# Performance work log

Measured on AMD Instinct MI355X. Metric: run time of the kernel, lower is better.

## Reference

```python
import jax, jax.numpy as jnp
import numpy as np

D_MODEL = 1024
N_HEAD = 16
HEAD_DIM = D_MODEL // N_HEAD
D_INNER = (int(D_MODEL * 2.0) + 7) // 8 * 8  # 2048
EPS = 1e-6


def setup_inputs() -> dict:
    key = jax.random.key(0)
    ks = jax.random.split(key, 8)
    B, T = 2, 2048
    s = 0.02
    return {
        "x": jax.random.normal(ks[0], (B, T, D_MODEL), dtype=jnp.float32),
        "ln1_w": jnp.ones((D_MODEL,), jnp.float32),
        "ln2_w": jnp.ones((D_MODEL,), jnp.float32),
        "qkv_w": jax.random.normal(ks[1], (3 * D_MODEL, D_MODEL), jnp.float32) * s,
        "o_w": jax.random.normal(ks[2], (D_MODEL, D_MODEL), jnp.float32) * s,
        "gate_w": jax.random.normal(ks[3], (D_INNER, D_MODEL), jnp.float32) * s,
        "up_w": jax.random.normal(ks[4], (D_INNER, D_MODEL), jnp.float32) * s,
        "down_w": jax.random.normal(ks[5], (D_MODEL, D_INNER), jnp.float32) * s,
    }


def _rmsnorm(x, w):
    xf = x.astype(jnp.float32)
    rms = jax.lax.rsqrt(jnp.mean(xf * xf, axis=-1, keepdims=True) + EPS)
    return (xf * rms).astype(x.dtype) * w


def _attention(x, qkv_w, o_w):
    B, T, D = x.shape
    qkv = (x @ qkv_w.T).reshape(B, T, 3, N_HEAD, HEAD_DIM)
    q, k, v = qkv[:, :, 0], qkv[:, :, 1], qkv[:, :, 2]  # [B,T,H,hd]
    scale = 1.0 / np.sqrt(HEAD_DIM)
    att = jnp.einsum("bqhd,bkhd->bhqk", q, k) * scale
    causal = jnp.tril(jnp.ones((T, T), dtype=bool))
    att = jnp.where(causal[None, None], att, -jnp.inf)
    att = jax.nn.softmax(att, axis=-1)
    y = jnp.einsum("bhqk,bkhd->bqhd", att, v).reshape(B, T, D)
    return y @ o_w.T


def _ffn(x, gate_w, up_w, down_w):
    g = jax.nn.silu(x @ gate_w.T)
    u = x @ up_w.T
    return (g * u) @ down_w.T


def reference(x, ln1_w, ln2_w, qkv_w, o_w, gate_w, up_w, down_w):
    x = x + _attention(_rmsnorm(x, ln1_w), qkv_w, o_w)
    x = x + _ffn(_rmsnorm(x, ln2_w), gate_w, up_w, down_w)
    return x
```

## Files before the change

kernel.cpp:

```cpp
#include <hip/hip_runtime.h>
#include <hip/hip_bf16.h>
#include <cstdint>

typedef __hip_bfloat16 bf16;
typedef __attribute__((ext_vector_type(8))) short bf16x8;
typedef __attribute__((ext_vector_type(4))) float f32x4;
typedef __attribute__((ext_vector_type(4))) int i32x4;

#define T_SEQ 2048
#define DMODEL 1024
#define NHEAD 16
#define DHEAD 64
#define MROWS 4096

typedef const __attribute__((address_space(1))) void* gas_ptr;
typedef __attribute__((address_space(3))) void* las_ptr;

static __device__ __forceinline__ f32x4 mfma16(bf16x8 a, bf16x8 b, f32x4 c) {
  return __builtin_amdgcn_mfma_f32_16x16x32_bf16(a, b, c, 0, 0, 0);
}
static __device__ __forceinline__ void gload_lds16(const void* g, void* l) {
  __builtin_amdgcn_global_load_lds((gas_ptr)g, (las_ptr)l, 16, 0, 0);
}
static __device__ __forceinline__ float b2f(unsigned short u) {
  union { unsigned int i; float f; } x; x.i = ((unsigned int)u) << 16; return x.f;
}
static __device__ __forceinline__ unsigned short f2bu(float f) {
  __hip_bfloat16 h = __float2bfloat16(f);
  unsigned short u; __builtin_memcpy(&u, &h, 2); return u;
}

__global__ __launch_bounds__(256) void f2ball_k(const float* __restrict__ a,
                                                const float* __restrict__ b,
                                                const float* __restrict__ c,
                                                const float* __restrict__ d,
                                                const float* __restrict__ e,
                                                bf16* __restrict__ out) {
  const int idx = (blockIdx.x * 256 + threadIdx.x) * 4;
  const float* src;
  int off;
  if (idx < 3145728)      { src = a; off = idx; }
  else if (idx < 4194304) { src = b; off = idx - 3145728; }
  else if (idx < 6291456) { src = c; off = idx - 4194304; }
  else if (idx < 8388608) { src = d; off = idx - 6291456; }
  else                    { src = e; off = idx - 8388608; }
  const float4 v = *(const float4*)(src + off);
  ushort4 ov;
  ov.x = f2bu(v.x); ov.y = f2bu(v.y); ov.z = f2bu(v.z); ov.w = f2bu(v.w);
  *(ushort4*)((unsigned short*)out + idx) = ov;
}

__global__ __launch_bounds__(256) void rms_k(const float* __restrict__ x,
                                             const float* __restrict__ w,
                                             bf16* __restrict__ out) {
  const int row = blockIdx.x;
  const int tid = threadIdx.x;
  const float4 v = ((const float4*)(x + (size_t)row * DMODEL))[tid];
  float ss = v.x * v.x + v.y * v.y + v.z * v.z + v.w * v.w;
#pragma unroll
  for (int off = 32; off; off >>= 1) ss += __shfl_xor(ss, off);
  __shared__ float red[4];
  if ((tid & 63) == 0) red[tid >> 6] = ss;
  __syncthreads();
  const float tot = red[0] + red[1] + red[2] + red[3];
  const float rinv = rsqrtf(tot * (1.f / DMODEL) + 1e-6f);
  const float4 wv = ((const float4*)w)[tid];
  bf16* o = out + (size_t)row * DMODEL + tid * 4;
  o[0] = __float2bfloat16(v.x * rinv * wv.x);
  o[1] = __float2bfloat16(v.y * rinv * wv.y);
  o[2] = __float2bfloat16(v.z * rinv * wv.z);
  o[3] = __float2bfloat16(v.w * rinv * wv.w);
}

template <int K, int EPI>
__global__ __launch_bounds__(256) void gemm_bt(const bf16* __restrict__ A,
                                               const bf16* __restrict__ Bw, int N,
                                               void* __restrict__ o0, void* __restrict__ o1,
                                               void* __restrict__ o2,
                                               const float* __restrict__ res) {
  __shared__ bf16 As[128 * 32];
  __shared__ bf16 Bs[128 * 32];
  const int bn0 = blockIdx.x * 128;
  const int bm0 = blockIdx.y * 128;
  const int tid = threadIdx.x;
  const int wave = tid >> 6, lane = tid & 63;
  const int wr = wave >> 1, wc = wave & 1;
  const int fr = lane & 15, g8 = (lane >> 4) * 8, r4 = (lane >> 4) * 4;
  const int srow = lane >> 2;
  const int scol = (lane & 3) * 8;

  const f32x4 fzero = {0.f, 0.f, 0.f, 0.f};
  f32x4 acc[4][4];
#pragma unroll
  for (int i = 0; i < 4; i++)
#pragma unroll
    for (int j = 0; j < 4; j++) acc[i][j] = fzero;

  const bf16* gA0 = A + (size_t)(bm0 + wave * 16 + srow) * K + scol;
  const bf16* gA1 = A + (size_t)(bm0 + (wave + 4) * 16 + srow) * K + scol;
  const bf16* gB0 = Bw + (size_t)(bn0 + wave * 16 + srow) * K + scol;
  const bf16* gB1 = Bw + (size_t)(bn0 + (wave + 4) * 16 + srow) * K + scol;

  for (int k0 = 0; k0 < K; k0 += 32) {
    gload_lds16(gA0 + k0, &As[wave * 512]);
    gload_lds16(gA1 + k0, &As[(wave + 4) * 512]);
    gload_lds16(gB0 + k0, &Bs[wave * 512]);
    gload_lds16(gB1 + k0, &Bs[(wave + 4) * 512]);
    __syncthreads();
    bf16x8 af[4], bfr[4];
#pragma unroll
    for (int mr = 0; mr < 4; mr++)
      af[mr] = *(const bf16x8*)&As[(wr * 64 + mr * 16 + fr) * 32 + g8];
#pragma unroll
    for (int nr = 0; nr < 4; nr++)
      bfr[nr] = *(const bf16x8*)&Bs[(wc * 64 + nr * 16 + fr) * 32 + g8];
#pragma unroll
    for (int mr = 0; mr < 4; mr++)
#pragma unroll
      for (int nr = 0; nr < 4; nr++)
        acc[mr][nr] = mfma16(af[mr], bfr[nr], acc[mr][nr]);
    __syncthreads();
  }

#pragma unroll
  for (int mr = 0; mr < 4; mr++) {
#pragma unroll
    for (int nr = 0; nr < 4; nr++) {
#pragma unroll
      for (int r = 0; r < 4; r++) {
        const int row = bm0 + wr * 64 + mr * 16 + r4 + r;
        const int col = bn0 + wc * 64 + nr * 16 + fr;
        const float vsum = acc[mr][nr][r];
        if (EPI == 0) {
          ((bf16*)o0)[(size_t)row * N + col] = __float2bfloat16(vsum);
        } else if (EPI == 1) {
          const int sel = col >> 10;
          const int n = col & 1023;
          const int h = n >> 6, d = n & 63;
          const int b = row >> 11, t = row & 2047;
          if (sel == 2) {
            ((bf16*)o2)[(((size_t)(b * NHEAD + h)) * DHEAD + d) * T_SEQ + t] =
                __float2bfloat16(vsum);
          } else {
            bf16* dst = (sel == 0) ? (bf16*)o0 : (bf16*)o1;
            dst[(((size_t)(b * NHEAD + h)) * T_SEQ + t) * DHEAD + d] = __float2bfloat16(vsum);
          }
        } else if (EPI == 2) {
          ((float*)o0)[(size_t)row * N + col] = res[(size_t)row * N + col] + vsum;
        } else {
          const int half = N >> 1;
          bf16* dst = (col < half) ? (bf16*)o0 : (bf16*)o1;
          const int c = (col < half) ? col : col - half;
          dst[(size_t)row * half + c] = __float2bfloat16(vsum);
        }
      }
    }
  }
}

__global__ __launch_bounds__(256) void attn_k(const bf16* __restrict__ qb,
                                              const bf16* __restrict__ kb,
                                              const bf16* __restrict__ vt,
                                              bf16* __restrict__ y,
                                              unsigned short* __restrict__ pO,
                                              float* __restrict__ pL) {
  const int wave = threadIdx.x >> 6, lane = threadIdx.x & 63;
  const int bid = blockIdx.x;
  int bh, qt, ks0, nb, heavy, hs;
  if (bid < 1024) {
    const int c = bid & 7, r = bid >> 3;
    bh = c * 4 + (r & 3);
    const int idx = r >> 2;
    qt = 31 - (idx >> 1);
    hs = idx & 1;
    heavy = 1;
    nb = qt + 1;
    ks0 = hs * nb;
  } else {
    const int bd = bid - 1024;
    const int c = bd & 7, r = bd >> 3;
    bh = c * 4 + (r & 3);
    qt = 15 - (r >> 2);
    hs = 0;
    heavy = 0;
    nb = 2 * qt + 2;
    ks0 = 0;
  }
  const int b = bh >> 4, h = bh & 15;
  const int fr = lane & 15, g8 = (lane >> 4) * 8, r4 = (lane >> 4) * 4;
  const int u = lane >> 4;
  const int src1 = fr + ((u & 1) << 5);
  const int src2 = src1 + 16;
  const bool hB = u >= 2;

  const bf16* qp = qb + (size_t)bh * T_SEQ * DHEAD;
  const bf16* kp = kb + (size_t)bh * T_SEQ * DHEAD;
  const bf16* vp = vt + (size_t)bh * DHEAD * T_SEQ;

  __shared__ char Ks[2][4096];
  __shared__ char Vs[2][4096];

  const int q0 = qt * 64 + wave * 16;
  const int kend = q0 + 16;
  const int qrow = q0 + fr;

  const bf16x8 qf0 = *(const bf16x8*)(qp + (size_t)(q0 + fr) * DHEAD + g8);
  const bf16x8 qf1 = *(const bf16x8*)(qp + (size_t)(q0 + fr) * DHEAD + 32 + g8);

  const int krow_l = lane >> 3;
  const int kslot_l = (lane & 7) ^ krow_l;
  const int vrow_l = lane >> 2;
  const int vslot_l = (lane & 3) ^ ((lane >> 3) & 3);

  const int kswz = (fr & 7) << 4;
  const int koffA = fr * 128 + ((u * 16) ^ kswz);
  const int koffB = fr * 128 + (((4 + u) * 16) ^ kswz);
  const int vswz = ((fr >> 1) & 3) << 4;

  const f32x4 fzero = {0.f, 0.f, 0.f, 0.f};
  f32x4 acc[4];
  float lpart = 0.f;
#pragma unroll
  for (int nf = 0; nf < 4; nf++) acc[nf] = fzero;

  gload_lds16(kp + (size_t)(ks0 * 32 + wave * 8 + krow_l) * DHEAD + kslot_l * 8,
              &Ks[0][wave * 1024]);
  gload_lds16(vp + (size_t)(wave * 16 + vrow_l) * T_SEQ + ks0 * 32 + vslot_l * 8,
              &Vs[0][wave * 1024]);
  __syncthreads();

  for (int ts = 0; ts < nb; ++ts) {
    const int kt = (ks0 + ts) * 32;
    const int buf = ts & 1;
    if (ts + 1 < nb) {
      const int kn = kt + 32;
      gload_lds16(kp + (size_t)(kn + wave * 8 + krow_l) * DHEAD + kslot_l * 8,
                  &Ks[buf ^ 1][wave * 1024]);
      gload_lds16(vp + (size_t)(wave * 16 + vrow_l) * T_SEQ + kn + vslot_l * 8,
                  &Vs[buf ^ 1][wave * 1024]);
    }
    if (kt < kend) {
      const char* KB = Ks[buf];
      const char* VB = Vs[buf];
      const bf16x8 kf0a = *(const bf16x8*)(KB + koffA);
      const bf16x8 kf0b = *(const bf16x8*)(KB + koffB);
      const bf16x8 kf1a = *(const bf16x8*)(KB + 2048 + koffA);
      const bf16x8 kf1b = *(const bf16x8*)(KB + 2048 + koffB);
      bf16x8 vf[4];
#pragma unroll
      for (int nf = 0; nf < 4; nf++)
        vf[nf] = *(const bf16x8*)(VB + (nf * 16 + fr) * 64 + ((u * 16) ^ vswz));

      f32x4 s0 = mfma16(kf0a, qf0, fzero);
      s0 = mfma16(kf0b, qf1, s0);
      f32x4 s1 = mfma16(kf1a, qf0, fzero);
      s1 = mfma16(kf1b, qf1, s1);

      float x0[4], x1[4];
      if (kt + 31 < q0) {
#pragma unroll
        for (int r = 0; r < 4; r++) {
          x0[r] = __expf(fminf(s0[r] * 0.125f, 30.f));
          x1[r] = __expf(fminf(s1[r] * 0.125f, 30.f));
          lpart += x0[r] + x1[r];
        }
      } else {
#pragma unroll
        for (int r = 0; r < 4; r++) {
          const int k0 = kt + r4 + r;
          const int k1 = k0 + 16;
          x0[r] = (k0 <= qrow) ? __expf(fminf(s0[r] * 0.125f, 30.f)) : 0.f;
          x1[r] = (k1 <= qrow) ? __expf(fminf(s1[r] * 0.125f, 30.f)) : 0.f;
          lpart += x0[r] + x1[r];
        }
      }

      const int A01 = (int)((unsigned)f2bu(x0[0]) | ((unsigned)f2bu(x0[1]) << 16));
      const int A23 = (int)((unsigned)f2bu(x0[2]) | ((unsigned)f2bu(x0[3]) << 16));
      const int B01 = (int)((unsigned)f2bu(x1[0]) | ((unsigned)f2bu(x1[1]) << 16));
      const int B23 = (int)((unsigned)f2bu(x1[2]) | ((unsigned)f2bu(x1[3]) << 16));

      const int t0a = __shfl(A01, src1), t0b = __shfl(B01, src1);
      const int t1a = __shfl(A23, src1), t1b = __shfl(B23, src1);
      const int t2a = __shfl(A01, src2), t2b = __shfl(B01, src2);
      const int t3a = __shfl(A23, src2), t3b = __shfl(B23, src2);
      i32x4 pw;
      pw[0] = hB ? t0b : t0a;
      pw[1] = hB ? t1b : t1a;
      pw[2] = hB ? t2b : t2a;
      pw[3] = hB ? t3b : t3a;
      const bf16x8 pb = __builtin_bit_cast(bf16x8, pw);

#pragma unroll
      for (int nf = 0; nf < 4; nf++) acc[nf] = mfma16(vf[nf], pb, acc[nf]);
    }
    __syncthreads();
  }

  lpart += __shfl_xor(lpart, 16);
  lpart += __shfl_xor(lpart, 32);

  if (!heavy) {
    const float inv = 1.f / lpart;
    const int t = q0 + fr;
    unsigned short* yb =
        (unsigned short*)(y + (((size_t)(b * T_SEQ + t)) * NHEAD + h) * DHEAD);
#pragma unroll
    for (int nf = 0; nf < 4; nf++) {
      ushort4 ov;
      ov.x = f2bu(acc[nf][0] * inv);
      ov.y = f2bu(acc[nf][1] * inv);
      ov.z = f2bu(acc[nf][2] * inv);
      ov.w = f2bu(acc[nf][3] * inv);
      *(ushort4*)(yb + nf * 16 + r4) = ov;
    }
  } else {
    const int tl = q0 - 1024 + fr;
    unsigned short* po = pO + ((size_t)(hs * 32 + bh) * 1024 + tl) * DHEAD;
#pragma unroll
    for (int nf = 0; nf < 4; nf++) {
      ushort4 ov;
      ov.x = f2bu(acc[nf][0]);
      ov.y = f2bu(acc[nf][1]);
      ov.z = f2bu(acc[nf][2]);
      ov.w = f2bu(acc[nf][3]);
      *(ushort4*)(po + nf * 16 + r4) = ov;
    }
    if (lane < 16) pL[(size_t)(hs * 32 + bh) * 1024 + (q0 - 1024) + lane] = lpart;
  }
}

__global__ __launch_bounds__(256) void comb_k(const unsigned short* __restrict__ pO,
                                              const float* __restrict__ pL,
                                              bf16* __restrict__ y) {
  const int idx = blockIdx.x * 256 + threadIdx.x;
  const int row = idx >> 4;
  const int d0 = (idx & 15) * 4;
  const int bh = row >> 10, tl = row & 1023;
  const int b = bh >> 4, h = bh & 15;
  const int t = 1024 + tl;
  const float inv = 1.f / (pL[row] + pL[32768 + row]);
  const ushort4 a = *(const ushort4*)(pO + (size_t)row * DHEAD + d0);
  const ushort4 c = *(const ushort4*)(pO + (size_t)(32768 + row) * DHEAD + d0);
  ushort4 ov;
  ov.x = f2bu((b2f(a.x) + b2f(c.x)) * inv);
  ov.y = f2bu((b2f(a.y) + b2f(c.y)) * inv);
  ov.z = f2bu((b2f(a.z) + b2f(c.z)) * inv);
  ov.w = f2bu((b2f(a.w) + b2f(c.w)) * inv);
  *(ushort4*)((unsigned short*)y + (((size_t)(b * T_SEQ + t)) * NHEAD + h) * DHEAD + d0) = ov;
}

__global__ void silumul_k(const bf16* __restrict__ g, const bf16* __restrict__ u,
                          bf16* __restrict__ o, int n) {
  const int idx = (blockIdx.x * blockDim.x + threadIdx.x) * 4;
  if (idx < n) {
    const ushort4 gv = *(const ushort4*)((const unsigned short*)g + idx);
    const ushort4 uv = *(const ushort4*)((const unsigned short*)u + idx);
    ushort4 ov;
    float a, s;
    a = b2f(gv.x); s = a / (1.f + __expf(-a)); ov.x = f2bu(s * b2f(uv.x));
    a = b2f(gv.y); s = a / (1.f + __expf(-a)); ov.y = f2bu(s * b2f(uv.y));
    a = b2f(gv.z); s = a / (1.f + __expf(-a)); ov.z = f2bu(s * b2f(uv.z));
    a = b2f(gv.w); s = a / (1.f + __expf(-a)); ov.w = f2bu(s * b2f(uv.w));
    *(ushort4*)((unsigned short*)o + idx) = ov;
  }
}

extern "C" void kernel_launch(void* const* d_in, const int* in_sizes, int n_in,
                              void* d_out, int out_size, void* d_ws, size_t ws_size,
                              hipStream_t stream) {
  const float* x     = (const float*)d_in[0];
  const float* ln1w  = (const float*)d_in[1];
  const float* ln2w  = (const float*)d_in[2];
  const float* qkvw  = (const float*)d_in[3];
  const float* ow    = (const float*)d_in[4];
  const float* gatew = (const float*)d_in[5];
  const float* upw   = (const float*)d_in[6];
  const float* downw = (const float*)d_in[7];

  uint8_t* ws = (uint8_t*)d_ws;
  bf16* WQKV = (bf16*)(ws + 0);
  bf16* WO   = (bf16*)(ws + 6291456);
  bf16* WG   = (bf16*)(ws + 8388608);
  bf16* WU   = (bf16*)(ws + 12582912);
  bf16* WD   = (bf16*)(ws + 16777216);
  bf16* H    = (bf16*)(ws + 20971520);
  bf16* Q    = (bf16*)(ws + 29360128);
  bf16* Kb   = (bf16*)(ws + 37748736);
  bf16* VT   = (bf16*)(ws + 46137344);
  bf16* Y    = (bf16*)(ws + 54525952);
  float* X2  = (float*)(ws + 62914560);
  bf16* G = (bf16*)(ws + 29360128);
  bf16* U = (bf16*)(ws + 46137344);
  unsigned short* pO = (unsigned short*)(ws + 62914560);
  float* pL = (float*)(ws + 20971520);

  f2ball_k<<<10240, 256, 0, stream>>>(qkvw, ow, gatew, upw, downw, (bf16*)ws);

  rms_k<<<MROWS, 256, 0, stream>>>(x, ln1w, H);
  gemm_bt<1024, 1><<<dim3(24, 32), 256, 0, stream>>>(H, WQKV, 3072, Q, Kb, VT, nullptr);
  attn_k<<<1536, 256, 0, stream>>>(Q, Kb, VT, Y, pO, pL);
  comb_k<<<2048, 256, 0, stream>>>(pO, pL, Y);
  gemm_bt<1024, 2><<<dim3(8, 32), 256, 0, stream>>>(Y, WO, 1024, X2, nullptr, nullptr, x);

  rms_k<<<MROWS, 256, 0, stream>>>(X2, ln2w, H);
  gemm_bt<1024, 3><<<dim3(32, 32), 256, 0, stream>>>(H, WG, 4096, G, U, nullptr, nullptr);
  silumul_k<<<8192, 256, 0, stream>>>(G, U, G, 4096 * 2048);
  gemm_bt<2048, 2><<<dim3(8, 32), 256, 0, stream>>>(G, WD, 1024, (float*)d_out, nullptr, nullptr, X2);
}
```

Before: 242.8 us.

## Fuse SiLU-multiply into gate/up GEMM epilogue with interleaved weights; XCD block swizzle

The weight conversion kernel now interleaves gate and up weight rows, so the combined GEMM emits gate and up values in adjacent output columns. The new GEMM epilogue exchanges each neighbouring pair with a lane shuffle, applies SiLU(g)*u and writes a single bf16 intermediate. This removes the separate silumul kernel and the write-then-reread of the G and U tensors. All GEMMs also remap workgroup IDs in groups of 8, so that tiles sharing operands land on the same XCD for better L2 reuse. The cost is that only half the lanes store in the fused epilogue, at a 2-element column stride.

```diff
diff --git a/kernel.cpp b/kernel.cpp
--- a/kernel.cpp
+++ b/kernel.cpp
@@ -38,16 +38,24 @@
                                                 bf16* __restrict__ out) {
   const int idx = (blockIdx.x * 256 + threadIdx.x) * 4;
   const float* src;
-  int off;
-  if (idx < 3145728)      { src = a; off = idx; }
-  else if (idx < 4194304) { src = b; off = idx - 3145728; }
-  else if (idx < 6291456) { src = c; off = idx - 4194304; }
-  else if (idx < 8388608) { src = d; off = idx - 6291456; }
-  else                    { src = e; off = idx - 8388608; }
+  int off, dst;
+  if (idx < 3145728) {
+    src = a; off = idx; dst = idx;
+  } else if (idx < 4194304) {
+    src = b; off = idx - 3145728; dst = idx;
+  } else if (idx < 6291456) {
+    src = c; off = idx - 4194304;
+    dst = 4194304 + ((off >> 10) << 11) + (off & 1023);
+  } else if (idx < 8388608) {
+    src = d; off = idx - 6291456;
+    dst = 4194304 + ((off >> 10) << 11) + 1024 + (off & 1023);
+  } else {
+    src = e; off = idx - 8388608; dst = idx;
+  }
   const float4 v = *(const float4*)(src + off);
   ushort4 ov;
   ov.x = f2bu(v.x); ov.y = f2bu(v.y); ov.z = f2bu(v.z); ov.w = f2bu(v.w);
-  *(ushort4*)((unsigned short*)out + idx) = ov;
+  *(ushort4*)((unsigned short*)out + dst) = ov;
 }
 
 __global__ __launch_bounds__(256) void rms_k(const float* __restrict__ x,
@@ -80,8 +88,12 @@
                                                const float* __restrict__ res) {
   __shared__ bf16 As[128 * 32];
   __shared__ bf16 Bs[128 * 32];
-  const int bn0 = blockIdx.x * 128;
-  const int bm0 = blockIdx.y * 128;
+  const int nbx = gridDim.x;
+  const int nwg = nbx * gridDim.y;
+  int fb = blockIdx.y * nbx + blockIdx.x;
+  fb = (fb & 7) * (nwg >> 3) + (fb >> 3);
+  const int bn0 = (fb % nbx) * 128;
+  const int bm0 = (fb / nbx) * 128;
   const int tid = threadIdx.x;
   const int wave = tid >> 6, lane = tid & 63;
   const int wr = wave >> 1, wc = wave & 1;
@@ -148,10 +160,13 @@
         } else if (EPI == 2) {
           ((float*)o0)[(size_t)row * N + col] = res[(size_t)row * N + col] + vsum;
         } else {
-          const int half = N >> 1;
-          bf16* dst = (col < half) ? (bf16*)o0 : (bf16*)o1;
-          const int c = (col < half) ? col : col - half;
-          dst[(size_t)row * half + c] = __float2bfloat16(vsum);
+          const float other = __shfl_xor(vsum, 1);
+          if ((fr & 1) == 0) {
+            const float g = vsum, u = other;
+            const float s = g / (1.f + __expf(-g));
+            ((bf16*)o0)[(size_t)row * (N >> 1) + (col >> 1)] =
+                __float2bfloat16(s * u);
+          }
         }
       }
     }
@@ -350,22 +365,6 @@
   *(ushort4*)((unsigned short*)y + (((size_t)(b * T_SEQ + t)) * NHEAD + h) * DHEAD + d0) = ov;
 }
 
-__global__ void silumul_k(const bf16* __restrict__ g, const bf16* __restrict__ u,
-                          bf16* __restrict__ o, int n) {
-  const int idx = (blockIdx.x * blockDim.x + threadIdx.x) * 4;
-  if (idx < n) {
-    const ushort4 gv = *(const ushort4*)((const unsigned short*)g + idx);
-    const ushort4 uv = *(const ushort4*)((const unsigned short*)u + idx);
-    ushort4 ov;
-    float a, s;
-    a = b2f(gv.x); s = a / (1.f + __expf(-a)); ov.x = f2bu(s * b2f(uv.x));
-    a = b2f(gv.y); s = a / (1.f + __expf(-a)); ov.y = f2bu(s * b2f(uv.y));
-    a = b2f(gv.z); s = a / (1.f + __expf(-a)); ov.z = f2bu(s * b2f(uv.z));
-    a = b2f(gv.w); s = a / (1.f + __expf(-a)); ov.w = f2bu(s * b2f(uv.w));
-    *(ushort4*)((unsigned short*)o + idx) = ov;
-  }
-}
-
 extern "C" void kernel_launch(void* const* d_in, const int* in_sizes, int n_in,
                               void* d_out, int out_size, void* d_ws, size_t ws_size,
                               hipStream_t stream) {
@@ -381,8 +380,7 @@
   uint8_t* ws = (uint8_t*)d_ws;
   bf16* WQKV = (bf16*)(ws + 0);
   bf16* WO   = (bf16*)(ws + 6291456);
-  bf16* WG   = (bf16*)(ws + 8388608);
-  bf16* WU   = (bf16*)(ws + 12582912);
+  bf16* WGU  = (bf16*)(ws + 8388608);
   bf16* WD   = (bf16*)(ws + 16777216);
   bf16* H    = (bf16*)(ws + 20971520);
   bf16* Q    = (bf16*)(ws + 29360128);
@@ -391,7 +389,6 @@
   bf16* Y    = (bf16*)(ws + 54525952);
   float* X2  = (float*)(ws + 62914560);
   bf16* G = (bf16*)(ws + 29360128);
-  bf16* U = (bf16*)(ws + 46137344);
   unsigned short* pO = (unsigned short*)(ws + 62914560);
   float* pL = (float*)(ws + 20971520);
 
@@ -404,7 +401,6 @@
   gemm_bt<1024, 2><<<dim3(8, 32), 256, 0, stream>>>(Y, WO, 1024, X2, nullptr, nullptr, x);
 
   rms_k<<<MROWS, 256, 0, stream>>>(X2, ln2w, H);
-  gemm_bt<1024, 3><<<dim3(32, 32), 256, 0, stream>>>(H, WG, 4096, G, U, nullptr, nullptr);
-  silumul_k<<<8192, 256, 0, stream>>>(G, U, G, 4096 * 2048);
+  gemm_bt<1024, 4><<<dim3(32, 32), 256, 0, stream>>>(H, WGU, 4096, G, nullptr, nullptr, nullptr);
   gemm_bt<2048, 2><<<dim3(8, 32), 256, 0, stream>>>(G, WD, 1024, (float*)d_out, nullptr, nullptr, X2);
 }
```

After: 234.6 us. 1.03x faster.
